# Kernel tuning notes

Measured on AMD Instinct MI355X. Metric: run time of the kernel, lower is better.

The kernel has to match this reference:

```python
import jax, jax.numpy as jnp
import numpy as np

BN_EPS = 1e-5
LRELU_SLOPE = 0.2


def _knn(x, k):
    # x: (B, C, N). Returns idx (B, N, k) of k nearest neighbors (incl. self).
    inner = -2.0 * jnp.einsum('bcn,bcm->bnm', x, x)          # (B, N, N)
    xx = jnp.sum(x * x, axis=1)                               # (B, N)
    dist = -xx[:, :, None] - inner - xx[:, None, :]           # negative sq. distance
    _, idx = jax.lax.top_k(dist, k)                           # (B, N, k)
    return idx


def setup_inputs() -> dict:
    key = jax.random.key(0)
    k1, k2 = jax.random.split(key)
    B, C, N, O, K = 8, 64, 4096, 64, 16
    x = jax.random.normal(k1, (B, C, N), dtype=jnp.float32)
    W = jax.random.normal(k2, (O, 2 * C), dtype=jnp.float32) * (1.0 / np.sqrt(2 * C))
    gamma = jnp.ones((O,), dtype=jnp.float32)
    beta = jnp.zeros((O,), dtype=jnp.float32)
    return {"x": x, "W": W, "gamma": gamma, "beta": beta, "k": K}


def reference(x, W, gamma, beta, k):
    # x: (B, C, N); W: (O, 2C) 1x1 conv weight; BN in training mode (batch stats).
    idx = _knn(x, k)                                          # (B, N, k) int32
    x_t = jnp.transpose(x, (0, 2, 1))                         # (B, N, C)
    neighbor = jax.vmap(lambda xt, i: xt[i])(x_t, idx)        # (B, N, k, C)
    center = x_t[:, :, None, :]                               # (B, N, 1, C)
    feat = jnp.concatenate(
        (neighbor - center, jnp.broadcast_to(center, neighbor.shape)), axis=-1
    )                                                         # (B, N, k, 2C)
    y = jnp.einsum('bnkc,oc->bonk', feat, W)                  # (B, O, N, k)
    # BatchNorm2d (training mode): stats over (B, N, k) per channel
    mean = jnp.mean(y, axis=(0, 2, 3), keepdims=True)
    var = jnp.var(y, axis=(0, 2, 3), keepdims=True)
    y = (y - mean) * jax.lax.rsqrt(var + BN_EPS)
    y = y * gamma[None, :, None, None] + beta[None, :, None, None]
    y = jnp.where(y >= 0, y, LRELU_SLOPE * y)                 # LeakyReLU(0.2)
    return jnp.max(y, axis=-1)                                # (B, O, N)
```

## Files before the change

### kernel.cpp

```cpp
#include <hip/hip_runtime.h>

#define NPTS 4096
#define NCH  64
#define NB   8
#define KNN  16

typedef _Float16 h8 __attribute__((ext_vector_type(8)));
typedef float    f4 __attribute__((ext_vector_type(4)));
typedef unsigned long long ull;

__global__ __launch_bounds__(256) void k_prep(const float* __restrict__ x,
                                              double* __restrict__ xx,
                                              _Float16* __restrict__ xhT,
                                              _Float16* __restrict__ xlT) {
    __shared__ float tile[64 * 65];
    const int tid = threadIdx.x;
    const int blk = blockIdx.x;
    const int b = blk >> 6, n0 = (blk & 63) << 6;
    const float* xb = x + (size_t)b * NCH * NPTS;
    for (int i = tid; i < 4096; i += 256) {
        int c = i >> 6, nn = i & 63;
        tile[c * 65 + nn] = xb[(size_t)c * NPTS + n0 + nn];
    }
    __syncthreads();
    if (tid < 64) {
        double a = 0.0;
        #pragma unroll
        for (int c = 0; c < 64; ++c) {
            double v = (double)tile[c * 65 + tid];
            a = fma(v, v, a);
        }
        xx[((size_t)b << 12) + n0 + tid] = a;
    }
    for (int i = tid; i < 4096; i += 256) {
        int n = i >> 6, c = i & 63;
        float v = tile[c * 65 + n];
        _Float16 h = (_Float16)v;
        _Float16 l = (_Float16)(v - (float)h);
        size_t o = (((size_t)b << 12) + n0 + n) * 64 + c;
        xhT[o] = h;
        xlT[o] = l;
    }
}

__global__ __launch_bounds__(256) void k_knn(const float* __restrict__ x,
                                             const double* __restrict__ xx,
                                             const _Float16* __restrict__ xhT,
                                             const _Float16* __restrict__ xlT,
                                             int* __restrict__ idx_out) {
    __shared__ __align__(16) char ldsbuf[34816];
    __shared__ int okflag;
    const int tid = threadIdx.x, lane = tid & 63, w = tid >> 6;
    const int g = lane >> 4, j = lane & 15;
    const int b = blockIdx.y, q0 = blockIdx.x * 64;
    const size_t bbase = (size_t)b << 12;
    const _Float16* Hb = xhT + bbase * 64;
    const _Float16* Lb = xlT + bbase * 64;
    const double*  xxb = xx + bbase;

    const int qcol = q0 + 16 * w + j;
    h8 Bh[2], Bl[2];
    #pragma unroll
    for (int kk = 0; kk < 2; ++kk) {
        size_t o = (size_t)qcol * 64 + kk * 32 + 8 * g;
        Bh[kk] = *(const h8*)(Hb + o);
        Bl[kk] = *(const h8*)(Lb + o);
    }

    if (tid == 0) okflag = 1;
    __syncthreads();

    {
        const int rsh = q0 + 16 * w + ((j + 1) & 15);
        f4 acc = {0.f, 0.f, 0.f, 0.f};
        #pragma unroll
        for (int kk = 0; kk < 2; ++kk) {
            size_t o = (size_t)rsh * 64 + kk * 32 + 8 * g;
            h8 Ah = *(const h8*)(Hb + o);
            h8 Al = *(const h8*)(Lb + o);
            acc = __builtin_amdgcn_mfma_f32_16x16x32_f16(Ah, Bh[kk], acc, 0, 0, 0);
            acc = __builtin_amdgcn_mfma_f32_16x16x32_f16(Ah, Bl[kk], acc, 0, 0, 0);
            acc = __builtin_amdgcn_mfma_f32_16x16x32_f16(Al, Bh[kk], acc, 0, 0, 0);
        }
        bool bad = false;
        #pragma unroll
        for (int rr = 0; rr < 2; ++rr) {
            const int r = rr ? 3 : 0;
            const int urow = q0 + 16 * w + ((4 * g + r + 1) & 15);
            double tgt = 0.0;
            #pragma unroll 4
            for (int c = 0; c < 64; ++c) {
                double av = (double)(float)Hb[(size_t)urow * 64 + c]
                          + (double)(float)Lb[(size_t)urow * 64 + c];
                double bv = (double)(float)Hb[(size_t)qcol * 64 + c]
                          + (double)(float)Lb[(size_t)qcol * 64 + c];
                tgt = fma(av, bv, tgt);
            }
            double got = (double)acc[r];
            if (fabs(got - tgt) > 1e-3 * (1.0 + fabs(tgt))) bad = true;
        }
        if (__any(bad ? 1 : 0)) okflag = 0;
    }
    __syncthreads();
    const bool mfma_ok = (okflag != 0);

    double s[16];
    #pragma unroll
    for (int i = 0; i < 16; ++i) s[i] = 0.0;

    if (mfma_ok) {
        for (int t = 0; t < 64; ++t) {
            const int m0 = t * 64;
            #pragma unroll
            for (int mt = 0; mt < 4; ++mt) {
                const int arow = m0 + 16 * mt + j;
                f4 acc = {0.f, 0.f, 0.f, 0.f};
                #pragma unroll
                for (int kk = 0; kk < 2; ++kk) {
                    size_t o = (size_t)arow * 64 + kk * 32 + 8 * g;
                    h8 Ah = *(const h8*)(Hb + o);
                    h8 Al = *(const h8*)(Lb + o);
                    acc = __builtin_amdgcn_mfma_f32_16x16x32_f16(Ah, Bh[kk], acc, 0, 0, 0);
                    acc = __builtin_amdgcn_mfma_f32_16x16x32_f16(Ah, Bl[kk], acc, 0, 0, 0);
                    acc = __builtin_amdgcn_mfma_f32_16x16x32_f16(Al, Bh[kk], acc, 0, 0, 0);
                }
                const int mbase = m0 + 16 * mt + 4 * g;
                #pragma unroll
                for (int r = 0; r < 4; ++r) {
                    const int m = mbase + r;
                    double dv = fma(2.0, (double)acc[r], -xxb[m]);
                    double pv = dv + 4096.0;
                    ull bits = (((ull)__double_as_longlong(pv)) & 0xFFFFFFFFFFFFF000ULL)
                             | (ull)(4095 - m);
                    double v = __longlong_as_double((long long)bits);
                    #pragma unroll
                    for (int i = 0; i < 15; ++i) s[i] = fmin(s[i + 1], fmax(v, s[i]));
                    s[15] = fmax(v, s[15]);
                }
            }
        }
    } else {
        float* fbQ = (float*)ldsbuf;
        float* fbM = ((float*)ldsbuf) + 64 * 66;
        const float* xb = x + (size_t)b * NCH * NPTS;
        for (int i = tid; i < 4096; i += 256) {
            int c = i >> 6, q = i & 63;
            fbQ[q * 66 + c] = xb[(size_t)c * NPTS + q0 + q];
        }
        for (int t = 0; t < 64; ++t) {
            const int m0 = t * 64;
            __syncthreads();
            for (int i = tid; i < 4096; i += 256) {
                int c = i >> 6, m = i & 63;
                fbM[m * 66 + c] = xb[(size_t)c * NPTS + m0 + m];
            }
            __syncthreads();
            const float* qp = fbQ + (16 * w + j) * 66;
            #pragma unroll
            for (int mt = 0; mt < 4; ++mt) {
                #pragma unroll
                for (int r = 0; r < 4; ++r) {
                    const int ml = 16 * mt + 4 * g + r, m = m0 + ml;
                    const float* mp = fbM + ml * 66;
                    double dot = 0.0;
                    #pragma unroll 8
                    for (int c = 0; c < 64; ++c)
                        dot = fma((double)qp[c], (double)mp[c], dot);
                    double dv = fma(2.0, dot, -xxb[m]);
                    double pv = dv + 4096.0;
                    ull bits = (((ull)__double_as_longlong(pv)) & 0xFFFFFFFFFFFFF000ULL)
                             | (ull)(4095 - m);
                    double v = __longlong_as_double((long long)bits);
                    #pragma unroll
                    for (int i = 0; i < 15; ++i) s[i] = fmin(s[i + 1], fmax(v, s[i]));
                    s[15] = fmax(v, s[15]);
                }
            }
        }
    }

    double* mg = (double*)ldsbuf;
    __syncthreads();
    #pragma unroll
    for (int i = 0; i < 16; ++i) mg[(size_t)tid * 17 + i] = s[i];
    __syncthreads();
    if (tid < 64) {
        double tb[16];
        #pragma unroll
        for (int i = 0; i < 16; ++i) tb[i] = 0.0;
        #pragma unroll
        for (int g2 = 0; g2 < 4; ++g2) {
            const double* src = mg + (size_t)(64 * (tid >> 4) + 16 * g2 + (tid & 15)) * 17;
            #pragma unroll
            for (int e = 0; e < 16; ++e) {
                double v = src[e];
                #pragma unroll
                for (int i = 0; i < 15; ++i) tb[i] = fmin(tb[i + 1], fmax(v, tb[i]));
                tb[15] = fmax(v, tb[15]);
            }
        }
        int* op = idx_out + (bbase + q0 + tid) * KNN;
        #pragma unroll
        for (int i = 0; i < 16; ++i) {
            int code = (int)((ull)__double_as_longlong(tb[i]) & 0xFFFULL);
            op[i] = 4095 - code;
        }
    }
}

__global__ __launch_bounds__(256) void k_pq(const float* __restrict__ x,
                                            const float* __restrict__ W,
                                            float* __restrict__ P,
                                            float* __restrict__ Q) {
    __shared__ __align__(16) float sX[4096];
    __shared__ __align__(16) float sWt[8192];
    const int tid = threadIdx.x;
    const int g0  = blockIdx.x * 64;
    const int b   = g0 >> 12;
    const int n0  = g0 & 4095;
    const float* xb = x + (size_t)b * NCH * NPTS;

    for (int i = tid; i < 8192; i += 256) {
        int c = i >> 7, oc = i & 127;
        float wv;
        if (oc < 64) wv = W[oc * 128 + c];
        else { int o = oc - 64; wv = W[o * 128 + 64 + c] - W[o * 128 + c]; }
        sWt[c * 128 + oc] = wv;
    }
    for (int i = tid; i < 4096; i += 256) {
        int c = i >> 6, m = i & 63;
        sX[i] = xb[(size_t)c * NPTS + n0 + m];
    }
    __syncthreads();

    const int ty = tid >> 4, tx = tid & 15;
    float aP[4][4], aQ[4][4];
    #pragma unroll
    for (int i = 0; i < 4; ++i)
        #pragma unroll
        for (int jj = 0; jj < 4; ++jj) { aP[i][jj] = 0.f; aQ[i][jj] = 0.f; }

    const float4* a4 = (const float4*)sX + ty;
    const float4* p4 = (const float4*)sWt + tx;
    const float4* q4 = (const float4*)sWt + 16 + tx;
    #pragma unroll 8
    for (int kk = 0; kk < 64; ++kk) {
        float4 a  = a4[kk * 16];
        float4 wp = p4[kk * 32];
        float4 wq = q4[kk * 32];
        aP[0][0] = fmaf(a.x, wp.x, aP[0][0]); aP[0][1] = fmaf(a.x, wp.y, aP[0][1]);
        aP[0][2] = fmaf(a.x, wp.z, aP[0][2]); aP[0][3] = fmaf(a.x, wp.w, aP[0][3]);
        aP[1][0] = fmaf(a.y, wp.x, aP[1][0]); aP[1][1] = fmaf(a.y, wp.y, aP[1][1]);
        aP[1][2] = fmaf(a.y, wp.z, aP[1][2]); aP[1][3] = fmaf(a.y, wp.w, aP[1][3]);
        aP[2][0] = fmaf(a.z, wp.x, aP[2][0]); aP[2][1] = fmaf(a.z, wp.y, aP[2][1]);
        aP[2][2] = fmaf(a.z, wp.z, aP[2][2]); aP[2][3] = fmaf(a.z, wp.w, aP[2][3]);
        aP[3][0] = fmaf(a.w, wp.x, aP[3][0]); aP[3][1] = fmaf(a.w, wp.y, aP[3][1]);
        aP[3][2] = fmaf(a.w, wp.z, aP[3][2]); aP[3][3] = fmaf(a.w, wp.w, aP[3][3]);
        aQ[0][0] = fmaf(a.x, wq.x, aQ[0][0]); aQ[0][1] = fmaf(a.x, wq.y, aQ[0][1]);
        aQ[0][2] = fmaf(a.x, wq.z, aQ[0][2]); aQ[0][3] = fmaf(a.x, wq.w, aQ[0][3]);
        aQ[1][0] = fmaf(a.y, wq.x, aQ[1][0]); aQ[1][1] = fmaf(a.y, wq.y, aQ[1][1]);
        aQ[1][2] = fmaf(a.y, wq.z, aQ[1][2]); aQ[1][3] = fmaf(a.y, wq.w, aQ[1][3]);
        aQ[2][0] = fmaf(a.z, wq.x, aQ[2][0]); aQ[2][1] = fmaf(a.z, wq.y, aQ[2][1]);
        aQ[2][2] = fmaf(a.z, wq.z, aQ[2][2]); aQ[2][3] = fmaf(a.z, wq.w, aQ[2][3]);
        aQ[3][0] = fmaf(a.w, wq.x, aQ[3][0]); aQ[3][1] = fmaf(a.w, wq.y, aQ[3][1]);
        aQ[3][2] = fmaf(a.w, wq.z, aQ[3][2]); aQ[3][3] = fmaf(a.w, wq.w, aQ[3][3]);
    }
    #pragma unroll
    for (int i = 0; i < 4; ++i) {
        size_t row = (size_t)(g0 + ty * 4 + i) * 64;
        float4 vp; vp.x = aP[i][0]; vp.y = aP[i][1]; vp.z = aP[i][2]; vp.w = aP[i][3];
        float4 vq; vq.x = aQ[i][0]; vq.y = aQ[i][1]; vq.z = aQ[i][2]; vq.w = aQ[i][3];
        ((float4*)(P + row))[tx] = vp;
        ((float4*)(Q + row))[tx] = vq;
    }
}

__global__ __launch_bounds__(256) void k_stats(const float* __restrict__ P,
                                               const float* __restrict__ Q,
                                               const int* __restrict__ idx,
                                               float* __restrict__ Mx,
                                               float* __restrict__ Mn,
                                               float* __restrict__ gsum,
                                               float* __restrict__ gsum2) {
    const int tid = threadIdx.x;
    const int o = tid & 63, ng = tid >> 6;
    const int b = blockIdx.y;
    const int n0 = blockIdx.x * 16;
    const float* Pb = P + (((size_t)b << 12) * 64);
    float ssum = 0.f, ssq = 0.f;
    for (int jj = 0; jj < 4; ++jj) {
        int n = n0 + ng * 4 + jj;
        size_t base = ((size_t)b << 12) + n;
        float qv = Q[base * 64 + o];
        const int* ip = idx + base * 16;
        float vmax = -3.4e38f, vmin = 3.4e38f;
        #pragma unroll
        for (int k = 0; k < 16; ++k) {
            int m = ip[k];
            float v = Pb[(size_t)m * 64 + o] + qv;
            vmax = fmaxf(vmax, v);
            vmin = fminf(vmin, v);
            ssum += v;
            ssq  = fmaf(v, v, ssq);
        }
        Mx[base * 64 + o] = vmax;
        Mn[base * 64 + o] = vmin;
    }
    __shared__ float red[8][64];
    red[ng][o] = ssum;
    red[ng + 4][o] = ssq;
    __syncthreads();
    if (tid < 64) {
        float ss  = red[0][o] + red[1][o] + red[2][o] + red[3][o];
        float ss2 = red[4][o] + red[5][o] + red[6][o] + red[7][o];
        atomicAdd(&gsum[o], ss);
        atomicAdd(&gsum2[o], ss2);
    }
}

__global__ __launch_bounds__(256) void k_final(const float* __restrict__ Mx,
                                               const float* __restrict__ Mn,
                                               const float* __restrict__ gsum,
                                               const float* __restrict__ gsum2,
                                               const float* __restrict__ gamma,
                                               const float* __restrict__ beta,
                                               float* __restrict__ out) {
    __shared__ float tX[64 * 65], tN[64 * 65];
    const int tid = threadIdx.x;
    const int b = blockIdx.y;
    const int n0 = blockIdx.x * 64;
    size_t base = ((size_t)b << 12) + n0;
    for (int i = tid; i < 4096; i += 256) {
        int nl = i >> 6, o = i & 63;
        tX[nl * 65 + o] = Mx[(base + nl) * 64 + o];
        tN[nl * 65 + o] = Mn[(base + nl) * 64 + o];
    }
    __syncthreads();
    const int lane = tid & 63, wv = tid >> 6;
    const float inv = 1.0f / 524288.0f;
    for (int oo = 0; oo < 16; ++oo) {
        int o = wv * 16 + oo;
        float mean = gsum[o] * inv;
        float var  = gsum2[o] * inv - mean * mean;
        float scv  = gamma[o] * rsqrtf(var + 1e-5f);
        float bsv  = beta[o] - mean * scv;
        float M = (scv >= 0.f) ? tX[lane * 65 + o] : tN[lane * 65 + o];
        float v = fmaf(scv, M, bsv);
        out[((size_t)b * 64 + o) * 4096 + n0 + lane] = (v >= 0.f) ? v : 0.2f * v;
    }
}

extern "C" void kernel_launch(void* const* d_in, const int* in_sizes, int n_in,
                              void* d_out, int out_size, void* d_ws, size_t ws_size,
                              hipStream_t stream) {
    const float* x     = (const float*)d_in[0];
    const float* W     = (const float*)d_in[1];
    const float* gamma = (const float*)d_in[2];
    const float* beta  = (const float*)d_in[3];
    float* out = (float*)d_out;

    char* ws = (char*)d_ws;
    double*    xx    = (double*)(ws);
    float*     gsum  = (float*)(ws + 262144);
    float*     gsum2 = (float*)(ws + 262400);
    int*       idx   = (int*)  (ws + 393216);
    _Float16*  xhT   = (_Float16*)(ws + 2490368);
    _Float16*  xlT   = (_Float16*)(ws + 6684672);
    float*     P     = (float*)(ws + 10878976);
    float*     Q     = (float*)(ws + 19267584);
    float*     Mx    = (float*)(ws + 2490368);
    float*     Mn    = (float*)(ws + 27656192);

    hipMemsetAsync(gsum, 0, 512, stream);
    k_prep <<<dim3(512),      256, 0, stream>>>(x, xx, xhT, xlT);
    k_knn  <<<dim3(64, 8),    256, 0, stream>>>(x, xx, xhT, xlT, idx);
    k_pq   <<<dim3(512),      256, 0, stream>>>(x, W, P, Q);
    k_stats<<<dim3(256, 8),   256, 0, stream>>>(P, Q, idx, Mx, Mn, gsum, gsum2);
    k_final<<<dim3(64, 8),    256, 0, stream>>>(Mx, Mn, gsum, gsum2, gamma, beta, out);
}
```

Baseline: 469.2 us.

## Split kNN candidate range across blocks and merge partial top-k lists

The kNN kernel now splits the 4096 candidate points into four chunks via a third grid dimension, so each block scans a quarter of the candidates and emits a partial top-16 per query. In-block merging uses wave shuffles instead of LDS, and a new merge kernel combines the four partial lists into final indices. The squared-norm bias is prefolded as 4096 minus the norm to save one add per candidate. This raises occupancy for the latency-bound insertion sort, at the cost of an extra kernel launch and a global buffer of partial results.

```diff
diff --git a/kernel.cpp b/kernel.cpp
--- a/kernel.cpp
+++ b/kernel.cpp
@@ -4,13 +4,14 @@
 #define NCH  64
 #define NB   8
 #define KNN  16
+#define NSPLIT 4
 
 typedef _Float16 h8 __attribute__((ext_vector_type(8)));
 typedef float    f4 __attribute__((ext_vector_type(4)));
 typedef unsigned long long ull;
 
 __global__ __launch_bounds__(256) void k_prep(const float* __restrict__ x,
-                                              double* __restrict__ xx,
+                                              double* __restrict__ xm,
                                               _Float16* __restrict__ xhT,
                                               _Float16* __restrict__ xlT) {
     __shared__ float tile[64 * 65];
@@ -30,7 +31,7 @@
             double v = (double)tile[c * 65 + tid];
             a = fma(v, v, a);
         }
-        xx[((size_t)b << 12) + n0 + tid] = a;
+        xm[((size_t)b << 12) + n0 + tid] = 4096.0 - a;
     }
     for (int i = tid; i < 4096; i += 256) {
         int n = i >> 6, c = i & 63;
@@ -44,19 +45,20 @@
 }
 
 __global__ __launch_bounds__(256) void k_knn(const float* __restrict__ x,
-                                             const double* __restrict__ xx,
+                                             const double* __restrict__ xm,
                                              const _Float16* __restrict__ xhT,
                                              const _Float16* __restrict__ xlT,
-                                             int* __restrict__ idx_out) {
-    __shared__ __align__(16) char ldsbuf[34816];
+                                             double* __restrict__ part) {
     __shared__ int okflag;
     const int tid = threadIdx.x, lane = tid & 63, w = tid >> 6;
     const int g = lane >> 4, j = lane & 15;
     const int b = blockIdx.y, q0 = blockIdx.x * 64;
+    const int split = blockIdx.z;
+    const int t0 = split * 16;
     const size_t bbase = (size_t)b << 12;
     const _Float16* Hb = xhT + bbase * 64;
     const _Float16* Lb = xlT + bbase * 64;
-    const double*  xxb = xx + bbase;
+    const double*  xmb = xm + bbase;
 
     const int qcol = q0 + 16 * w + j;
     h8 Bh[2], Bl[2];
@@ -109,7 +111,7 @@
     for (int i = 0; i < 16; ++i) s[i] = 0.0;
 
     if (mfma_ok) {
-        for (int t = 0; t < 64; ++t) {
+        for (int t = t0; t < t0 + 16; ++t) {
             const int m0 = t * 64;
             #pragma unroll
             for (int mt = 0; mt < 4; ++mt) {
@@ -128,8 +130,7 @@
                 #pragma unroll
                 for (int r = 0; r < 4; ++r) {
                     const int m = mbase + r;
-                    double dv = fma(2.0, (double)acc[r], -xxb[m]);
-                    double pv = dv + 4096.0;
+                    double pv = fma(2.0, (double)acc[r], xmb[m]);
                     ull bits = (((ull)__double_as_longlong(pv)) & 0xFFFFFFFFFFFFF000ULL)
                              | (ull)(4095 - m);
                     double v = __longlong_as_double((long long)bits);
@@ -140,34 +141,19 @@
             }
         }
     } else {
-        float* fbQ = (float*)ldsbuf;
-        float* fbM = ((float*)ldsbuf) + 64 * 66;
         const float* xb = x + (size_t)b * NCH * NPTS;
-        for (int i = tid; i < 4096; i += 256) {
-            int c = i >> 6, q = i & 63;
-            fbQ[q * 66 + c] = xb[(size_t)c * NPTS + q0 + q];
-        }
-        for (int t = 0; t < 64; ++t) {
+        for (int t = t0; t < t0 + 16; ++t) {
             const int m0 = t * 64;
-            __syncthreads();
-            for (int i = tid; i < 4096; i += 256) {
-                int c = i >> 6, m = i & 63;
-                fbM[m * 66 + c] = xb[(size_t)c * NPTS + m0 + m];
-            }
-            __syncthreads();
-            const float* qp = fbQ + (16 * w + j) * 66;
             #pragma unroll
             for (int mt = 0; mt < 4; ++mt) {
                 #pragma unroll
                 for (int r = 0; r < 4; ++r) {
-                    const int ml = 16 * mt + 4 * g + r, m = m0 + ml;
-                    const float* mp = fbM + ml * 66;
+                    const int m = m0 + 16 * mt + 4 * g + r;
                     double dot = 0.0;
-                    #pragma unroll 8
                     for (int c = 0; c < 64; ++c)
-                        dot = fma((double)qp[c], (double)mp[c], dot);
-                    double dv = fma(2.0, dot, -xxb[m]);
-                    double pv = dv + 4096.0;
+                        dot = fma((double)xb[(size_t)c * NPTS + m],
+                                  (double)xb[(size_t)c * NPTS + qcol], dot);
+                    double pv = fma(2.0, dot, xmb[m]);
                     ull bits = (((ull)__double_as_longlong(pv)) & 0xFFFFFFFFFFFFF000ULL)
                              | (ull)(4095 - m);
                     double v = __longlong_as_double((long long)bits);
@@ -179,32 +165,52 @@
         }
     }
 
-    double* mg = (double*)ldsbuf;
-    __syncthreads();
-    #pragma unroll
-    for (int i = 0; i < 16; ++i) mg[(size_t)tid * 17 + i] = s[i];
-    __syncthreads();
-    if (tid < 64) {
-        double tb[16];
-        #pragma unroll
-        for (int i = 0; i < 16; ++i) tb[i] = 0.0;
-        #pragma unroll
-        for (int g2 = 0; g2 < 4; ++g2) {
-            const double* src = mg + (size_t)(64 * (tid >> 4) + 16 * g2 + (tid & 15)) * 17;
-            #pragma unroll
-            for (int e = 0; e < 16; ++e) {
-                double v = src[e];
-                #pragma unroll
-                for (int i = 0; i < 15; ++i) tb[i] = fmin(tb[i + 1], fmax(v, tb[i]));
-                tb[15] = fmax(v, tb[15]);
-            }
-        }
-        int* op = idx_out + (bbase + q0 + tid) * KNN;
+    #pragma unroll
+    for (int i = 0; i < 16; ++i) {
+        double v = __shfl(s[i], (lane + 32) & 63, 64);
+        if (g < 2) {
+            #pragma unroll
+            for (int k2 = 0; k2 < 15; ++k2) s[k2] = fmin(s[k2 + 1], fmax(v, s[k2]));
+            s[15] = fmax(v, s[15]);
+        }
+    }
+    #pragma unroll
+    for (int i = 0; i < 16; ++i) {
+        double v = __shfl(s[i], (lane + 16) & 63, 64);
+        if (g == 0) {
+            #pragma unroll
+            for (int k2 = 0; k2 < 15; ++k2) s[k2] = fmin(s[k2 + 1], fmax(v, s[k2]));
+            s[15] = fmax(v, s[15]);
+        }
+    }
+    if (g == 0) {
+        const size_t qi = bbase + q0 + 16 * w + j;
+        #pragma unroll
+        for (int i = 0; i < 16; ++i)
+            part[(size_t)(split * 16 + i) * (NB * NPTS) + qi] = s[i];
+    }
+}
+
+__global__ __launch_bounds__(256) void k_kmerge(const double* __restrict__ part,
+                                                int* __restrict__ idx_out) {
+    const int qi = blockIdx.x * 256 + threadIdx.x;
+    double tb[16];
+    #pragma unroll
+    for (int i = 0; i < 16; ++i) tb[i] = 0.0;
+    for (int sp = 0; sp < NSPLIT; ++sp) {
         #pragma unroll
         for (int i = 0; i < 16; ++i) {
-            int code = (int)((ull)__double_as_longlong(tb[i]) & 0xFFFULL);
-            op[i] = 4095 - code;
-        }
+            double v = part[(size_t)(sp * 16 + i) * (NB * NPTS) + qi];
+            #pragma unroll
+            for (int k2 = 0; k2 < 15; ++k2) tb[k2] = fmin(tb[k2 + 1], fmax(v, tb[k2]));
+            tb[15] = fmax(v, tb[15]);
+        }
+    }
+    int* op = idx_out + (size_t)qi * KNN;
+    #pragma unroll
+    for (int i = 0; i < 16; ++i) {
+        int code = (int)((ull)__double_as_longlong(tb[i]) & 0xFFFULL);
+        op[i] = 4095 - code;
     }
 }
 
@@ -360,7 +366,7 @@
     float* out = (float*)d_out;
 
     char* ws = (char*)d_ws;
-    double*    xx    = (double*)(ws);
+    double*    xm    = (double*)(ws);
     float*     gsum  = (float*)(ws + 262144);
     float*     gsum2 = (float*)(ws + 262400);
     int*       idx   = (int*)  (ws + 393216);
@@ -368,13 +374,15 @@
     _Float16*  xlT   = (_Float16*)(ws + 6684672);
     float*     P     = (float*)(ws + 10878976);
     float*     Q     = (float*)(ws + 19267584);
+    double*    part  = (double*)(ws + 10878976);
     float*     Mx    = (float*)(ws + 2490368);
     float*     Mn    = (float*)(ws + 27656192);
 
     hipMemsetAsync(gsum, 0, 512, stream);
-    k_prep <<<dim3(512),      256, 0, stream>>>(x, xx, xhT, xlT);
-    k_knn  <<<dim3(64, 8),    256, 0, stream>>>(x, xx, xhT, xlT, idx);
-    k_pq   <<<dim3(512),      256, 0, stream>>>(x, W, P, Q);
-    k_stats<<<dim3(256, 8),   256, 0, stream>>>(P, Q, idx, Mx, Mn, gsum, gsum2);
-    k_final<<<dim3(64, 8),    256, 0, stream>>>(Mx, Mn, gsum, gsum2, gamma, beta, out);
-}
+    k_prep  <<<dim3(512),        256, 0, stream>>>(x, xm, xhT, xlT);
+    k_knn   <<<dim3(64, 8, 4),   256, 0, stream>>>(x, xm, xhT, xlT, part);
+    k_kmerge<<<dim3(128),        256, 0, stream>>>(part, idx);
+    k_pq    <<<dim3(512),        256, 0, stream>>>(x, W, P, Q);
+    k_stats <<<dim3(256, 8),     256, 0, stream>>>(P, Q, idx, Mx, Mn, gsum, gsum2);
+    k_final <<<dim3(64, 8),      256, 0, stream>>>(Mx, Mn, gsum, gsum2, gamma, beta, out);
+}
```

Measured after the change: 529.9 us. 1.13x slower.
